# Kernel optimization log

Hardware: AMD Instinct MI355X
Metric: run time of the kernel (lower is better)

Reference implementation:

```python
import jax, jax.numpy as jnp
import numpy as np

N = 100000
E = 1600000
IN_DIM, H1, H2, H3 = 128, 128, 64, 32


def gcn_conv(x, edge_index, W, b, n):
    # PyG GCNConv (default): add self-loops, symmetric norm D^-1/2 (A+I) D^-1/2,
    # out[dst] = sum_{src->dst} norm * (x @ W)[src] + b
    src, dst = edge_index[0], edge_index[1]
    loops = jnp.arange(n)
    src = jnp.concatenate([src, loops])
    dst = jnp.concatenate([dst, loops])
    deg = jax.ops.segment_sum(jnp.ones((src.shape[0],), dtype=x.dtype), dst, num_segments=n)
    dinv = jnp.where(deg > 0, jax.lax.rsqrt(deg), jnp.zeros((), dtype=x.dtype))
    norm = dinv[src] * dinv[dst]  # [E+N]
    h = x @ W                      # [N, out_dim] dense transform first (out_dim <= in_dim)
    msg = h[src] * norm[:, None]   # [E+N, out_dim] gather + scale
    out = jax.ops.segment_sum(msg, dst, num_segments=n)
    return out + b


def setup_inputs() -> dict:
    key = jax.random.key(0)
    ks = jax.random.split(key, 10)
    def glorot(k, shape):
        lim = np.sqrt(6.0 / (shape[0] + shape[1]))
        return jax.random.uniform(k, shape, jnp.float32, -lim, lim)
    return {
        "x": jax.random.normal(ks[0], (N, IN_DIM), jnp.float32),
        "edge_index": jax.random.randint(ks[1], (2, E), 0, N, jnp.int64),
        "W1": glorot(ks[2], (IN_DIM, H1)), "b1": jnp.zeros((H1,), jnp.float32),
        "W2": glorot(ks[3], (H1, H2)),     "b2": jnp.zeros((H2,), jnp.float32),
        "W3": glorot(ks[4], (H2, H3)),     "b3": jnp.zeros((H3,), jnp.float32),
        "Wl": glorot(ks[5], (H3, 1)),      "bl": jnp.zeros((1,), jnp.float32),
    }


def reference(x, edge_index, W1, b1, W2, b2, W3, b3, Wl, bl):
    n = x.shape[0]
    h = jax.nn.relu(gcn_conv(x, edge_index, W1, b1, n))   # dropout p=0.5 is identity in eval
    h = jax.nn.relu(gcn_conv(h, edge_index, W2, b2, n))
    h = jax.nn.relu(gcn_conv(h, edge_index, W3, b3, n))
    return jax.nn.sigmoid(h @ Wl + bl)                    # [N, 1]
```

## Files before the change

### kernel.cpp

```cpp
#include <hip/hip_runtime.h>
#include <hip/hip_fp16.h>
#include <math.h>


#define BSHIFT 9
#define BNODES (1 << BSHIFT)
#define SRCBITS 17

union H8 { float4 f4; __half2 h2[4]; };

typedef _Float16 half8 __attribute__((ext_vector_type(8)));
typedef float floatx4 __attribute__((ext_vector_type(4)));


__global__ __launch_bounds__(256) void k_hist(const int* __restrict__ dst, int E,
                                              int* __restrict__ bucketcnt, int B) {
    __shared__ int h[256];
    int tid = threadIdx.x;
    h[tid] = 0;
    __syncthreads();
    for (int i = blockIdx.x * 256 + tid; i < E; i += gridDim.x * 256)
        atomicAdd(&h[dst[i] >> BSHIFT], 1);
    __syncthreads();
    if (tid < B && h[tid] > 0) atomicAdd(&bucketcnt[tid], h[tid]);
}

__global__ __launch_bounds__(256) void k_bscan(const int* __restrict__ bucketcnt,
                                               int* __restrict__ bucketbase,
                                               int* __restrict__ bucketfill,
                                               int* __restrict__ row_ptr,
                                               int B, int n, int E) {
    __shared__ int s[256];
    int tid = threadIdx.x;
    int v = (tid < B) ? bucketcnt[tid] : 0;
    s[tid] = v;
    __syncthreads();
    for (int off = 1; off < 256; off <<= 1) {
        int t = (tid >= off) ? s[tid - off] : 0;
        __syncthreads();
        s[tid] += t;
        __syncthreads();
    }
    int excl = s[tid] - v;
    if (tid < B) { bucketbase[tid] = excl; bucketfill[tid] = excl; }
    if (tid == 0) { bucketbase[B] = E; row_ptr[n] = E; }
}

__global__ __launch_bounds__(256) void k_bucket(const int* __restrict__ src,
                                                const int* __restrict__ dst, int E,
                                                int* __restrict__ bucketfill,
                                                unsigned int* __restrict__ edgebuf,
                                                int B) {
    __shared__ int h[256];
    __shared__ int cursor[256];
    int tid = threadIdx.x;
    int base = blockIdx.x * 8192;
    int end = min(base + 8192, E);
    h[tid] = 0;
    __syncthreads();
    for (int i = base + tid; i < end; i += 256)
        atomicAdd(&h[dst[i] >> BSHIFT], 1);
    __syncthreads();
    if (tid < B) cursor[tid] = (h[tid] > 0) ? atomicAdd(&bucketfill[tid], h[tid]) : 0;
    __syncthreads();
    for (int i = base + tid; i < end; i += 256) {
        int d = dst[i];
        int b = d >> BSHIFT;
        unsigned int pk = ((unsigned int)(d & (BNODES - 1)) << SRCBITS) | (unsigned int)src[i];
        int pos = atomicAdd(&cursor[b], 1);
        edgebuf[pos] = pk;
    }
}

__global__ __launch_bounds__(256) void k_build(const unsigned int* __restrict__ edgebuf,
                                               const int* __restrict__ bucketbase,
                                               int* __restrict__ row_ptr,
                                               float* __restrict__ dinv,
                                               int* __restrict__ col, int n) {
    __shared__ int cnt[BNODES];
    __shared__ int s[256];
    int b = blockIdx.x;
    int tid = threadIdx.x;
    int node0 = b << BSHIFT;
    int ebase = bucketbase[b], eend = bucketbase[b + 1];
    cnt[tid] = 0;
    cnt[tid + 256] = 0;
    __syncthreads();
    for (int i = ebase + tid; i < eend; i += 256)
        atomicAdd(&cnt[edgebuf[i] >> SRCBITS], 1);
    __syncthreads();
    int c0 = cnt[2 * tid], c1 = cnt[2 * tid + 1];
    int tsum = c0 + c1;
    s[tid] = tsum;
    __syncthreads();
    for (int off = 1; off < 256; off <<= 1) {
        int t = (tid >= off) ? s[tid - off] : 0;
        __syncthreads();
        s[tid] += t;
        __syncthreads();
    }
    int excl = s[tid] - tsum;
    int pA = ebase + excl, pB = ebase + excl + c0;
    int nodeA = node0 + 2 * tid, nodeB = nodeA + 1;
    cnt[2 * tid] = pA;
    cnt[2 * tid + 1] = pB;
    if (nodeA < n) { row_ptr[nodeA] = pA; dinv[nodeA] = rsqrtf((float)(c0 + 1)); }
    if (nodeB < n) { row_ptr[nodeB] = pB; dinv[nodeB] = rsqrtf((float)(c1 + 1)); }
    __syncthreads();
    for (int i = ebase + tid; i < eend; i += 256) {
        unsigned int pk = edgebuf[i];
        int dl = pk >> SRCBITS;
        int sv = (int)(pk & ((1u << SRCBITS) - 1));
        int pos = atomicAdd(&cnt[dl], 1);
        col[pos] = sv;
    }
}

__global__ void k_packW(const float* __restrict__ W, _Float16* __restrict__ Wpk,
                        int IN, int OUT) {
    int e = blockIdx.x * 256 + threadIdx.x;
    if (e >= IN * OUT) return;
    int j = e & 7;
    int lane = (e >> 3) & 63;
    int rest = e >> 9;
    int NT = OUT >> 4;
    int t = rest % NT;
    int s = rest / NT;
    int k = s * 32 + (lane >> 4) * 8 + j;
    int nn = t * 16 + (lane & 15);
    Wpk[e] = (_Float16)W[k * OUT + nn];
}

template <int IN, int OUT, bool XHALF>
__global__ __launch_bounds__(256) void k_matmul_mfma(const void* __restrict__ xv,
                                                     const _Float16* __restrict__ Wpk,
                                                     const float* __restrict__ dinv,
                                                     __half* __restrict__ out, int n) {
    constexpr int S = IN / 32;
    constexpr int NT = OUT / 16;
    constexpr int LDH = IN + 8;
    __shared__ _Float16 xs[64 * LDH];

    int tid = threadIdx.x;
    int rowbase = blockIdx.x * 64;

    constexpr int TOT = 64 * IN / 8;
    const float4* x4 = (const float4*)xv;
    for (int i = tid; i < TOT; i += 256) {
        int r = i / (IN / 8), kg = i % (IN / 8);
        int row = rowbase + r;
        if (XHALF) {
            float4 v = make_float4(0.f, 0.f, 0.f, 0.f);
            if (row < n) v = x4[(size_t)row * (IN / 8) + kg];
            *(float4*)&xs[r * LDH + kg * 8] = v;
        } else {
            float4 a = make_float4(0.f, 0.f, 0.f, 0.f), b = a;
            if (row < n) {
                a = x4[(size_t)row * (IN / 4) + kg * 2 + 0];
                b = x4[(size_t)row * (IN / 4) + kg * 2 + 1];
            }
            _Float16* p = &xs[r * LDH + kg * 8];
            p[0] = (_Float16)a.x; p[1] = (_Float16)a.y;
            p[2] = (_Float16)a.z; p[3] = (_Float16)a.w;
            p[4] = (_Float16)b.x; p[5] = (_Float16)b.y;
            p[6] = (_Float16)b.z; p[7] = (_Float16)b.w;
        }
    }
    __syncthreads();

    int lane = tid & 63;
    int wave = tid >> 6;
    int m = lane & 15, quad = lane >> 4;

    floatx4 acc[NT];
#pragma unroll
    for (int t = 0; t < NT; ++t) acc[t] = (floatx4){0.f, 0.f, 0.f, 0.f};

    const half8* Wf = (const half8*)Wpk;
#pragma unroll
    for (int s = 0; s < S; ++s) {
        half8 a = *(const half8*)&xs[(wave * 16 + m) * LDH + s * 32 + quad * 8];
#pragma unroll
        for (int t = 0; t < NT; ++t) {
            half8 b = Wf[(s * NT + t) * 64 + lane];
            acc[t] = __builtin_amdgcn_mfma_f32_16x16x32_f16(a, b, acc[t], 0, 0, 0);
        }
    }

    int rbase = rowbase + wave * 16 + quad * 4;
#pragma unroll
    for (int r = 0; r < 4; ++r) {
        int row = rbase + r;
        if (row < n) {
            float dsc = dinv[row];
#pragma unroll
            for (int t = 0; t < NT; ++t)
                out[(size_t)row * OUT + t * 16 + m] = __float2half(acc[t][r] * dsc);
        }
    }
}

template <int F, bool RELU>
__global__ __launch_bounds__(256) void k_aggregate_h(const __half* __restrict__ hs,
                                                     const float* __restrict__ dinv,
                                                     const float* __restrict__ bias,
                                                     const int* __restrict__ row_ptr,
                                                     const int* __restrict__ col,
                                                     __half* __restrict__ out, int n) {
    constexpr int LPN = F / 8;
    int t = blockIdx.x * 256 + threadIdx.x;
    int node = t / LPN;
    int fg = t % LPN;
    if (node >= n) return;

    const float4* h4 = (const float4*)hs;
    float acc[8];
    {
        H8 u;
        u.f4 = h4[(size_t)node * LPN + fg];
#pragma unroll
        for (int q = 0; q < 4; ++q) {
            float2 f = __half22float2(u.h2[q]);
            acc[2 * q + 0] = f.x;
            acc[2 * q + 1] = f.y;
        }
    }
    int beg = row_ptr[node], end = row_ptr[node + 1];
    int j = beg;
    for (; j + 3 < end; j += 4) {
        int s0 = col[j], s1 = col[j + 1], s2 = col[j + 2], s3 = col[j + 3];
        H8 u0, u1, u2, u3;
        u0.f4 = h4[(size_t)s0 * LPN + fg];
        u1.f4 = h4[(size_t)s1 * LPN + fg];
        u2.f4 = h4[(size_t)s2 * LPN + fg];
        u3.f4 = h4[(size_t)s3 * LPN + fg];
#pragma unroll
        for (int q = 0; q < 4; ++q) {
            float2 f0 = __half22float2(u0.h2[q]);
            float2 f1 = __half22float2(u1.h2[q]);
            float2 f2 = __half22float2(u2.h2[q]);
            float2 f3 = __half22float2(u3.h2[q]);
            acc[2 * q + 0] += (f0.x + f1.x) + (f2.x + f3.x);
            acc[2 * q + 1] += (f0.y + f1.y) + (f2.y + f3.y);
        }
    }
    for (; j < end; ++j) {
        H8 u;
        u.f4 = h4[(size_t)col[j] * LPN + fg];
#pragma unroll
        for (int q = 0; q < 4; ++q) {
            float2 f = __half22float2(u.h2[q]);
            acc[2 * q + 0] += f.x;
            acc[2 * q + 1] += f.y;
        }
    }
    float dsc = dinv[node];
    H8 o;
#pragma unroll
    for (int q = 0; q < 4; ++q) {
        float v0 = fmaf(acc[2 * q + 0], dsc, bias[fg * 8 + 2 * q + 0]);
        float v1 = fmaf(acc[2 * q + 1], dsc, bias[fg * 8 + 2 * q + 1]);
        if (RELU) { v0 = fmaxf(v0, 0.f); v1 = fmaxf(v1, 0.f); }
        o.h2[q] = __floats2half2_rn(v0, v1);
    }
    ((float4*)out)[(size_t)node * LPN + fg] = o.f4;
}

__global__ void k_final(const __half* __restrict__ z, const float* __restrict__ Wl,
                        const float* __restrict__ bl, float* __restrict__ out, int n) {
    int i = blockIdx.x * blockDim.x + threadIdx.x;
    if (i >= n) return;
    const float4* z4 = (const float4*)(z + (size_t)i * 32);
    float acc = bl[0];
#pragma unroll
    for (int k = 0; k < 4; ++k) {
        H8 u;
        u.f4 = z4[k];
#pragma unroll
        for (int q = 0; q < 4; ++q) {
            float2 f = __half22float2(u.h2[q]);
            acc += f.x * Wl[k * 8 + 2 * q + 0] + f.y * Wl[k * 8 + 2 * q + 1];
        }
    }
    out[i] = 1.f / (1.f + expf(-acc));
}

extern "C" void kernel_launch(void* const* d_in, const int* in_sizes, int n_in,
                              void* d_out, int out_size, void* d_ws, size_t ws_size,
                              hipStream_t stream) {
    const float* x  = (const float*)d_in[0];
    const int*   ei = (const int*)d_in[1];
    const float* W1 = (const float*)d_in[2];
    const float* b1 = (const float*)d_in[3];
    const float* W2 = (const float*)d_in[4];
    const float* b2 = (const float*)d_in[5];
    const float* W3 = (const float*)d_in[6];
    const float* b3 = (const float*)d_in[7];
    const float* Wl = (const float*)d_in[8];
    const float* bl = (const float*)d_in[9];

    const int N = in_sizes[0] / 128;
    const int E = in_sizes[1] / 2;
    const int* src = ei;
    const int* dst = ei + E;
    const int B = (N + BNODES - 1) >> BSHIFT;

    char* ws = (char*)d_ws;
    size_t off = 0;
    auto take = [&](size_t bytes) -> char* {
        char* p = ws + off;
        off += (bytes + 255) & ~(size_t)255;
        return p;
    };
    int*          bucketcnt  = (int*)take(256 * 4);
    int*          bucketbase = (int*)take(257 * 4);
    int*          bucketfill = (int*)take(256 * 4);
    unsigned int* edgebuf    = (unsigned int*)take((size_t)E * 4);
    int*          row_ptr    = (int*)take((size_t)(N + 1) * 4);
    float*        dinv       = (float*)take((size_t)N * 4);
    int*          col        = (int*)take((size_t)E * 4);
    __half*       bufA       = (__half*)take((size_t)N * 128 * 2);
    __half*       bufB       = (__half*)take((size_t)N * 128 * 2);
    _Float16*     Wpk1       = (_Float16*)take(128 * 128 * 2);
    _Float16*     Wpk2       = (_Float16*)take(128 * 64 * 2);
    _Float16*     Wpk3       = (_Float16*)take(64 * 32 * 2);
    (void)ws_size;

    hipMemsetAsync(bucketcnt, 0, 256 * 4, stream);

    int gN = (N + 255) / 256;
    int gM = (N + 63) / 64;

    k_hist<<<512, 256, 0, stream>>>(dst, E, bucketcnt, B);
    k_bscan<<<1, 256, 0, stream>>>(bucketcnt, bucketbase, bucketfill, row_ptr, B, N, E);
    k_bucket<<<(E + 8191) / 8192, 256, 0, stream>>>(src, dst, E, bucketfill, edgebuf, B);
    k_build<<<B, 256, 0, stream>>>(edgebuf, bucketbase, row_ptr, dinv, col, N);

    k_packW<<<(128 * 128 + 255) / 256, 256, 0, stream>>>(W1, Wpk1, 128, 128);
    k_packW<<<(128 * 64 + 255) / 256, 256, 0, stream>>>(W2, Wpk2, 128, 64);
    k_packW<<<(64 * 32 + 255) / 256, 256, 0, stream>>>(W3, Wpk3, 64, 32);

    k_matmul_mfma<128, 128, false><<<gM, 256, 0, stream>>>(x, Wpk1, dinv, bufA, N);
    k_aggregate_h<128, true><<<((size_t)N * 16 + 255) / 256, 256, 0, stream>>>(
        bufA, dinv, b1, row_ptr, col, bufB, N);

    k_matmul_mfma<128, 64, true><<<gM, 256, 0, stream>>>(bufB, Wpk2, dinv, bufA, N);
    k_aggregate_h<64, true><<<((size_t)N * 8 + 255) / 256, 256, 0, stream>>>(
        bufA, dinv, b2, row_ptr, col, bufB, N);

    k_matmul_mfma<64, 32, true><<<gM, 256, 0, stream>>>(bufB, Wpk3, dinv, bufA, N);
    k_aggregate_h<32, true><<<((size_t)N * 4 + 255) / 256, 256, 0, stream>>>(
        bufA, dinv, b3, row_ptr, col, bufB, N);

    k_final<<<gN, 256, 0, stream>>>(bufB, Wl, bl, (float*)d_out, N);
}
```

Before: 319.9 us.

## Fuse aggregation with next-layer MFMA matmul and final linear layer

Each layer's neighbour aggregation now writes its relu output to shared memory, and the next layer's dense transform runs there with MFMA, so the intermediate half buffer no longer makes a global round trip and one launch per layer is saved. The last aggregation also computes the 32-to-1 linear layer and sigmoid using warp shuffles. The three weight-packing launches are merged into one. The CSR build switches to 256-node buckets with up to 512 buckets, and the bucketing chunk becomes 4096 edges. The risk is that the gather phase inside the fused kernel now runs with only 64 nodes per block, which may hide memory latency less well.

Measured after the change: 295.0 us. 7.8% less time.

```diff
diff --git a/kernel.cpp b/kernel.cpp
--- a/kernel.cpp
+++ b/kernel.cpp
@@ -3,9 +3,10 @@
 #include <math.h>
 
 
-#define BSHIFT 9
+#define BSHIFT 8
 #define BNODES (1 << BSHIFT)
 #define SRCBITS 17
+#define MAXB 512
 
 union H8 { float4 f4; __half2 h2[4]; };
 
@@ -15,27 +16,29 @@
 
 __global__ __launch_bounds__(256) void k_hist(const int* __restrict__ dst, int E,
                                               int* __restrict__ bucketcnt, int B) {
-    __shared__ int h[256];
-    int tid = threadIdx.x;
-    h[tid] = 0;
+    __shared__ int h[MAXB];
+    int tid = threadIdx.x;
+    h[tid] = 0; h[tid + 256] = 0;
     __syncthreads();
     for (int i = blockIdx.x * 256 + tid; i < E; i += gridDim.x * 256)
         atomicAdd(&h[dst[i] >> BSHIFT], 1);
     __syncthreads();
     if (tid < B && h[tid] > 0) atomicAdd(&bucketcnt[tid], h[tid]);
-}
-
-__global__ __launch_bounds__(256) void k_bscan(const int* __restrict__ bucketcnt,
+    int t2 = tid + 256;
+    if (t2 < B && h[t2] > 0) atomicAdd(&bucketcnt[t2], h[t2]);
+}
+
+__global__ __launch_bounds__(512) void k_bscan(const int* __restrict__ bucketcnt,
                                                int* __restrict__ bucketbase,
                                                int* __restrict__ bucketfill,
                                                int* __restrict__ row_ptr,
                                                int B, int n, int E) {
-    __shared__ int s[256];
+    __shared__ int s[MAXB];
     int tid = threadIdx.x;
     int v = (tid < B) ? bucketcnt[tid] : 0;
     s[tid] = v;
     __syncthreads();
-    for (int off = 1; off < 256; off <<= 1) {
+    for (int off = 1; off < MAXB; off <<= 1) {
         int t = (tid >= off) ? s[tid - off] : 0;
         __syncthreads();
         s[tid] += t;
@@ -51,17 +54,19 @@
                                                 int* __restrict__ bucketfill,
                                                 unsigned int* __restrict__ edgebuf,
                                                 int B) {
-    __shared__ int h[256];
-    __shared__ int cursor[256];
-    int tid = threadIdx.x;
-    int base = blockIdx.x * 8192;
-    int end = min(base + 8192, E);
-    h[tid] = 0;
+    __shared__ int h[MAXB];
+    __shared__ int cursor[MAXB];
+    int tid = threadIdx.x;
+    int base = blockIdx.x * 4096;
+    int end = min(base + 4096, E);
+    h[tid] = 0; h[tid + 256] = 0;
     __syncthreads();
     for (int i = base + tid; i < end; i += 256)
         atomicAdd(&h[dst[i] >> BSHIFT], 1);
     __syncthreads();
     if (tid < B) cursor[tid] = (h[tid] > 0) ? atomicAdd(&bucketfill[tid], h[tid]) : 0;
+    int t2 = tid + 256;
+    if (t2 < B) cursor[t2] = (h[t2] > 0) ? atomicAdd(&bucketfill[t2], h[t2]) : 0;
     __syncthreads();
     for (int i = base + tid; i < end; i += 256) {
         int d = dst[i];
@@ -78,20 +83,18 @@
                                                float* __restrict__ dinv,
                                                int* __restrict__ col, int n) {
     __shared__ int cnt[BNODES];
-    __shared__ int s[256];
+    __shared__ int s[BNODES];
     int b = blockIdx.x;
     int tid = threadIdx.x;
     int node0 = b << BSHIFT;
     int ebase = bucketbase[b], eend = bucketbase[b + 1];
     cnt[tid] = 0;
-    cnt[tid + 256] = 0;
     __syncthreads();
     for (int i = ebase + tid; i < eend; i += 256)
         atomicAdd(&cnt[edgebuf[i] >> SRCBITS], 1);
     __syncthreads();
-    int c0 = cnt[2 * tid], c1 = cnt[2 * tid + 1];
-    int tsum = c0 + c1;
-    s[tid] = tsum;
+    int c = cnt[tid];
+    s[tid] = c;
     __syncthreads();
     for (int off = 1; off < 256; off <<= 1) {
         int t = (tid >= off) ? s[tid - off] : 0;
@@ -99,40 +102,40 @@
         s[tid] += t;
         __syncthreads();
     }
-    int excl = s[tid] - tsum;
-    int pA = ebase + excl, pB = ebase + excl + c0;
-    int nodeA = node0 + 2 * tid, nodeB = nodeA + 1;
-    cnt[2 * tid] = pA;
-    cnt[2 * tid + 1] = pB;
-    if (nodeA < n) { row_ptr[nodeA] = pA; dinv[nodeA] = rsqrtf((float)(c0 + 1)); }
-    if (nodeB < n) { row_ptr[nodeB] = pB; dinv[nodeB] = rsqrtf((float)(c1 + 1)); }
+    int p = ebase + s[tid] - c;
+    int node = node0 + tid;
+    if (node < n) { row_ptr[node] = p; dinv[node] = rsqrtf((float)(c + 1)); }
+    cnt[tid] = p;
     __syncthreads();
     for (int i = ebase + tid; i < eend; i += 256) {
         unsigned int pk = edgebuf[i];
-        int dl = pk >> SRCBITS;
-        int sv = (int)(pk & ((1u << SRCBITS) - 1));
-        int pos = atomicAdd(&cnt[dl], 1);
-        col[pos] = sv;
-    }
-}
-
-__global__ void k_packW(const float* __restrict__ W, _Float16* __restrict__ Wpk,
-                        int IN, int OUT) {
+        int pos = atomicAdd(&cnt[pk >> SRCBITS], 1);
+        col[pos] = (int)(pk & ((1u << SRCBITS) - 1));
+    }
+}
+
+__global__ void k_packW3(const float* __restrict__ W1, const float* __restrict__ W2,
+                         const float* __restrict__ W3, _Float16* __restrict__ P1,
+                         _Float16* __restrict__ P2, _Float16* __restrict__ P3) {
     int e = blockIdx.x * 256 + threadIdx.x;
-    if (e >= IN * OUT) return;
-    int j = e & 7;
-    int lane = (e >> 3) & 63;
-    int rest = e >> 9;
+    const float* W; _Float16* P; int OUT, idx;
+    if (e < 16384)      { W = W1; P = P1; OUT = 128; idx = e; }
+    else if (e < 24576) { W = W2; P = P2; OUT = 64;  idx = e - 16384; }
+    else if (e < 26624) { W = W3; P = P3; OUT = 32;  idx = e - 24576; }
+    else return;
+    int j = idx & 7;
+    int lane = (idx >> 3) & 63;
+    int rest = idx >> 9;
     int NT = OUT >> 4;
     int t = rest % NT;
-    int s = rest / NT;
-    int k = s * 32 + (lane >> 4) * 8 + j;
+    int ss = rest / NT;
+    int k = ss * 32 + (lane >> 4) * 8 + j;
     int nn = t * 16 + (lane & 15);
-    Wpk[e] = (_Float16)W[k * OUT + nn];
-}
-
-template <int IN, int OUT, bool XHALF>
-__global__ __launch_bounds__(256) void k_matmul_mfma(const void* __restrict__ xv,
+    P[idx] = (_Float16)W[k * OUT + nn];
+}
+
+template <int IN, int OUT>
+__global__ __launch_bounds__(256) void k_matmul_mfma(const float* __restrict__ x,
                                                      const _Float16* __restrict__ Wpk,
                                                      const float* __restrict__ dinv,
                                                      __half* __restrict__ out, int n) {
@@ -145,26 +148,20 @@
     int rowbase = blockIdx.x * 64;
 
     constexpr int TOT = 64 * IN / 8;
-    const float4* x4 = (const float4*)xv;
+    const float4* x4 = (const float4*)x;
     for (int i = tid; i < TOT; i += 256) {
         int r = i / (IN / 8), kg = i % (IN / 8);
         int row = rowbase + r;
-        if (XHALF) {
-            float4 v = make_float4(0.f, 0.f, 0.f, 0.f);
-            if (row < n) v = x4[(size_t)row * (IN / 8) + kg];
-            *(float4*)&xs[r * LDH + kg * 8] = v;
-        } else {
-            float4 a = make_float4(0.f, 0.f, 0.f, 0.f), b = a;
-            if (row < n) {
-                a = x4[(size_t)row * (IN / 4) + kg * 2 + 0];
-                b = x4[(size_t)row * (IN / 4) + kg * 2 + 1];
-            }
-            _Float16* p = &xs[r * LDH + kg * 8];
-            p[0] = (_Float16)a.x; p[1] = (_Float16)a.y;
-            p[2] = (_Float16)a.z; p[3] = (_Float16)a.w;
-            p[4] = (_Float16)b.x; p[5] = (_Float16)b.y;
-            p[6] = (_Float16)b.z; p[7] = (_Float16)b.w;
-        }
+        float4 a = make_float4(0.f, 0.f, 0.f, 0.f), b = a;
+        if (row < n) {
+            a = x4[(size_t)row * (IN / 4) + kg * 2 + 0];
+            b = x4[(size_t)row * (IN / 4) + kg * 2 + 1];
+        }
+        _Float16* p = &xs[r * LDH + kg * 8];
+        p[0] = (_Float16)a.x; p[1] = (_Float16)a.y;
+        p[2] = (_Float16)a.z; p[3] = (_Float16)a.w;
+        p[4] = (_Float16)b.x; p[5] = (_Float16)b.y;
+        p[6] = (_Float16)b.z; p[7] = (_Float16)b.w;
     }
     __syncthreads();
 
@@ -200,14 +197,123 @@
     }
 }
 
-template <int F, bool RELU>
-__global__ __launch_bounds__(256) void k_aggregate_h(const __half* __restrict__ hs,
-                                                     const float* __restrict__ dinv,
-                                                     const float* __restrict__ bias,
-                                                     const int* __restrict__ row_ptr,
-                                                     const int* __restrict__ col,
-                                                     __half* __restrict__ out, int n) {
+template <int F, int OUT>
+__global__ __launch_bounds__(256) void k_agg_mm(const __half* __restrict__ hs,
+                                                const float* __restrict__ dinv,
+                                                const float* __restrict__ bias,
+                                                const int* __restrict__ row_ptr,
+                                                const int* __restrict__ col,
+                                                const _Float16* __restrict__ Wpk,
+                                                __half* __restrict__ out, int n) {
+    constexpr int S = F / 32;
+    constexpr int NT = OUT / 16;
+    constexpr int LDH = F + 8;
     constexpr int LPN = F / 8;
+    __shared__ _Float16 zs[64 * LDH];
+
+    int tid = threadIdx.x;
+    int rowbase = blockIdx.x * 64;
+    const float4* h4 = (const float4*)hs;
+
+    for (int task = tid; task < 64 * LPN; task += 256) {
+        int nl = task / LPN;
+        int fg = task % LPN;
+        int node = rowbase + nl;
+        H8 o;
+        if (node < n) {
+            float acc[8];
+            H8 u;
+            u.f4 = h4[(size_t)node * LPN + fg];
+#pragma unroll
+            for (int q = 0; q < 4; ++q) {
+                float2 f = __half22float2(u.h2[q]);
+                acc[2 * q + 0] = f.x;
+                acc[2 * q + 1] = f.y;
+            }
+            int beg = row_ptr[node], end = row_ptr[node + 1];
+            int j = beg;
+            for (; j + 3 < end; j += 4) {
+                int s0 = col[j], s1 = col[j + 1], s2 = col[j + 2], s3 = col[j + 3];
+                H8 u0, u1, u2, u3;
+                u0.f4 = h4[(size_t)s0 * LPN + fg];
+                u1.f4 = h4[(size_t)s1 * LPN + fg];
+                u2.f4 = h4[(size_t)s2 * LPN + fg];
+                u3.f4 = h4[(size_t)s3 * LPN + fg];
+#pragma unroll
+                for (int q = 0; q < 4; ++q) {
+                    float2 f0 = __half22float2(u0.h2[q]);
+                    float2 f1 = __half22float2(u1.h2[q]);
+                    float2 f2 = __half22float2(u2.h2[q]);
+                    float2 f3 = __half22float2(u3.h2[q]);
+                    acc[2 * q + 0] += (f0.x + f1.x) + (f2.x + f3.x);
+                    acc[2 * q + 1] += (f0.y + f1.y) + (f2.y + f3.y);
+                }
+            }
+            for (; j < end; ++j) {
+                H8 u2;
+                u2.f4 = h4[(size_t)col[j] * LPN + fg];
+#pragma unroll
+                for (int q = 0; q < 4; ++q) {
+                    float2 f = __half22float2(u2.h2[q]);
+                    acc[2 * q + 0] += f.x;
+                    acc[2 * q + 1] += f.y;
+                }
+            }
+            float dsc = dinv[node];
+#pragma unroll
+            for (int q = 0; q < 4; ++q) {
+                float v0 = fmaxf(fmaf(acc[2 * q + 0], dsc, bias[fg * 8 + 2 * q + 0]), 0.f);
+                float v1 = fmaxf(fmaf(acc[2 * q + 1], dsc, bias[fg * 8 + 2 * q + 1]), 0.f);
+                o.h2[q] = __floats2half2_rn(v0, v1);
+            }
+        } else {
+            o.f4 = make_float4(0.f, 0.f, 0.f, 0.f);
+        }
+        *(float4*)&zs[nl * LDH + fg * 8] = o.f4;
+    }
+    __syncthreads();
+
+    int lane = tid & 63;
+    int wave = tid >> 6;
+    int m = lane & 15, quad = lane >> 4;
+
+    floatx4 acc[NT];
+#pragma unroll
+    for (int t = 0; t < NT; ++t) acc[t] = (floatx4){0.f, 0.f, 0.f, 0.f};
+
+    const half8* Wf = (const half8*)Wpk;
+#pragma unroll
+    for (int s = 0; s < S; ++s) {
+        half8 a = *(const half8*)&zs[(wave * 16 + m) * LDH + s * 32 + quad * 8];
+#pragma unroll
+        for (int t = 0; t < NT; ++t) {
+            half8 b = Wf[(s * NT + t) * 64 + lane];
+            acc[t] = __builtin_amdgcn_mfma_f32_16x16x32_f16(a, b, acc[t], 0, 0, 0);
+        }
+    }
+
+    int rbase = rowbase + wave * 16 + quad * 4;
+#pragma unroll
+    for (int r = 0; r < 4; ++r) {
+        int row = rbase + r;
+        if (row < n) {
+            float dsc = dinv[row];
+#pragma unroll
+            for (int t = 0; t < NT; ++t)
+                out[(size_t)row * OUT + t * 16 + m] = __float2half(acc[t][r] * dsc);
+        }
+    }
+}
+
+__global__ __launch_bounds__(256) void k_agg_final(const __half* __restrict__ hs,
+                                                   const float* __restrict__ dinv,
+                                                   const float* __restrict__ bias,
+                                                   const int* __restrict__ row_ptr,
+                                                   const int* __restrict__ col,
+                                                   const float* __restrict__ Wl,
+                                                   const float* __restrict__ bl,
+                                                   float* __restrict__ out, int n) {
+    constexpr int LPN = 4;
     int t = blockIdx.x * 256 + threadIdx.x;
     int node = t / LPN;
     int fg = t % LPN;
@@ -255,34 +361,15 @@
         }
     }
     float dsc = dinv[node];
-    H8 o;
-#pragma unroll
-    for (int q = 0; q < 4; ++q) {
-        float v0 = fmaf(acc[2 * q + 0], dsc, bias[fg * 8 + 2 * q + 0]);
-        float v1 = fmaf(acc[2 * q + 1], dsc, bias[fg * 8 + 2 * q + 1]);
-        if (RELU) { v0 = fmaxf(v0, 0.f); v1 = fmaxf(v1, 0.f); }
-        o.h2[q] = __floats2half2_rn(v0, v1);
-    }
-    ((float4*)out)[(size_t)node * LPN + fg] = o.f4;
-}
-
-__global__ void k_final(const __half* __restrict__ z, const float* __restrict__ Wl,
-                        const float* __restrict__ bl, float* __restrict__ out, int n) {
-    int i = blockIdx.x * blockDim.x + threadIdx.x;
-    if (i >= n) return;
-    const float4* z4 = (const float4*)(z + (size_t)i * 32);
-    float acc = bl[0];
-#pragma unroll
-    for (int k = 0; k < 4; ++k) {
-        H8 u;
-        u.f4 = z4[k];
-#pragma unroll
-        for (int q = 0; q < 4; ++q) {
-            float2 f = __half22float2(u.h2[q]);
-            acc += f.x * Wl[k * 8 + 2 * q + 0] + f.y * Wl[k * 8 + 2 * q + 1];
-        }
-    }
-    out[i] = 1.f / (1.f + expf(-acc));
+    float partial = 0.f;
+#pragma unroll
+    for (int k = 0; k < 8; ++k) {
+        float v = fmaxf(fmaf(acc[k], dsc, bias[fg * 8 + k]), 0.f);
+        partial = fmaf(v, Wl[fg * 8 + k], partial);
+    }
+    partial += __shfl_xor(partial, 1);
+    partial += __shfl_xor(partial, 2);
+    if (fg == 0) out[node] = 1.f / (1.f + expf(-(partial + bl[0])));
 }
 
 extern "C" void kernel_launch(void* const* d_in, const int* in_sizes, int n_in,
@@ -312,9 +399,9 @@
         off += (bytes + 255) & ~(size_t)255;
         return p;
     };
-    int*          bucketcnt  = (int*)take(256 * 4);
-    int*          bucketbase = (int*)take(257 * 4);
-    int*          bucketfill = (int*)take(256 * 4);
+    int*          bucketcnt  = (int*)take(MAXB * 4);
+    int*          bucketbase = (int*)take((MAXB + 1) * 4);
+    int*          bucketfill = (int*)take(MAXB * 4);
     unsigned int* edgebuf    = (unsigned int*)take((size_t)E * 4);
     int*          row_ptr    = (int*)take((size_t)(N + 1) * 4);
     float*        dinv       = (float*)take((size_t)N * 4);
@@ -326,31 +413,23 @@
     _Float16*     Wpk3       = (_Float16*)take(64 * 32 * 2);
     (void)ws_size;
 
-    hipMemsetAsync(bucketcnt, 0, 256 * 4, stream);
-
-    int gN = (N + 255) / 256;
+    hipMemsetAsync(bucketcnt, 0, MAXB * 4, stream);
+
     int gM = (N + 63) / 64;
 
     k_hist<<<512, 256, 0, stream>>>(dst, E, bucketcnt, B);
-    k_bscan<<<1, 256, 0, stream>>>(bucketcnt, bucketbase, bucketfill, row_ptr, B, N, E);
-    k_bucket<<<(E + 8191) / 8192, 256, 0, stream>>>(src, dst, E, bucketfill, edgebuf, B);
+    k_bscan<<<1, MAXB, 0, stream>>>(bucketcnt, bucketbase, bucketfill, row_ptr, B, N, E);
+    k_bucket<<<(E + 4095) / 4096, 256, 0, stream>>>(src, dst, E, bucketfill, edgebuf, B);
     k_build<<<B, 256, 0, stream>>>(edgebuf, bucketbase, row_ptr, dinv, col, N);
 
-    k_packW<<<(128 * 128 + 255) / 256, 256, 0, stream>>>(W1, Wpk1, 128, 128);
-    k_packW<<<(128 * 64 + 255) / 256, 256, 0, stream>>>(W2, Wpk2, 128, 64);
-    k_packW<<<(64 * 32 + 255) / 256, 256, 0, stream>>>(W3, Wpk3, 64, 32);
-
-    k_matmul_mfma<128, 128, false><<<gM, 256, 0, stream>>>(x, Wpk1, dinv, bufA, N);
-    k_aggregate_h<128, true><<<((size_t)N * 16 + 255) / 256, 256, 0, stream>>>(
-        bufA, dinv, b1, row_ptr, col, bufB, N);
-
-    k_matmul_mfma<128, 64, true><<<gM, 256, 0, stream>>>(bufB, Wpk2, dinv, bufA, N);
-    k_aggregate_h<64, true><<<((size_t)N * 8 + 255) / 256, 256, 0, stream>>>(
-        bufA, dinv, b2, row_ptr, col, bufB, N);
-
-    k_matmul_mfma<64, 32, true><<<gM, 256, 0, stream>>>(bufB, Wpk3, dinv, bufA, N);
-    k_aggregate_h<32, true><<<((size_t)N * 4 + 255) / 256, 256, 0, stream>>>(
-        bufA, dinv, b3, row_ptr, col, bufB, N);
-
-    k_final<<<gN, 256, 0, stream>>>(bufB, Wl, bl, (float*)d_out, N);
-}
+    k_packW3<<<(26624 + 255) / 256, 256, 0, stream>>>(W1, W2, W3, Wpk1, Wpk2, Wpk3);
+
+    k_matmul_mfma<128, 128><<<gM, 256, 0, stream>>>(x, Wpk1, dinv, bufA, N);
+
+    k_agg_mm<128, 64><<<gM, 256, 0, stream>>>(bufA, dinv, b1, row_ptr, col, Wpk2, bufB, N);
+
+    k_agg_mm<64, 32><<<gM, 256, 0, stream>>>(bufB, dinv, b2, row_ptr, col, Wpk3, bufA, N);
+
+    k_agg_final<<<((size_t)N * 4 + 255) / 256, 256, 0, stream>>>(
+        bufA, dinv, b3, row_ptr, col, Wl, bl, (float*)d_out, N);
+}
```
